# Kernel optimization log

Hardware: AMD Instinct MI355X
Metric: run time of the kernel (lower is better)

## Reference

```python
import jax, jax.numpy as jnp
import numpy as np

B, MAX_N, MAX_E, MAX_BETA = 16, 512, 1024, 64
NODE_F, HID = 2, 128

def setup_inputs() -> dict:
    key = jax.random.key(0)
    ks = jax.random.split(key, 20)
    inp = {}
    inp["x"] = jax.random.normal(ks[0], (B, MAX_N, NODE_F), dtype=jnp.float32)
    inp["SCB"] = jax.random.normal(ks[1], (B, MAX_BETA, MAX_E), dtype=jnp.float32)
    inp["edge_index"] = jax.random.randint(ks[2], (B, 2, MAX_E), 0, MAX_N, dtype=jnp.int32)
    inp["edge_len"] = jax.random.randint(ks[3], (B,), 1, MAX_E + 1, dtype=jnp.int32)
    inp["beta_len"] = jax.random.randint(ks[4], (B,), 1, MAX_BETA + 1, dtype=jnp.int32)
    def lin(k, fi, fo):
        s = 1.0 / np.sqrt(fi)
        kw, kb = jax.random.split(k)
        return (jax.random.uniform(kw, (fi, fo), jnp.float32, -s, s),
                jax.random.uniform(kb, (fo,), jnp.float32, -s, s))
    inp["W1"], inp["b1"] = lin(ks[5], 4, 64)
    inp["W2"], inp["b2"] = lin(ks[6], 64, 64)
    inp["W3"], inp["b3"] = lin(ks[7], 64 + 4, 128)
    inp["W4"], inp["b4"] = lin(ks[8], 128, 128)
    inp["W5"], inp["b5"] = lin(ks[9], 128, HID)
    inp["W6"], inp["b6"] = lin(ks[10], HID, HID)
    return inp

def reference(x, SCB, edge_index, edge_len, beta_len,
              W1, b1, W2, b2, W3, b3, W4, b4, W5, b5, W6, b6):
    Bb, beta, E = SCB.shape
    SCBa = jnp.abs(SCB)  # torch.abs(he[2].to_dense())
    edge_mask = jnp.arange(E)[None, :] < edge_len[:, None]      # [B,E]
    beta_mask = jnp.arange(beta)[None, :] < beta_len[:, None]   # [B,beta]
    # e_feat = x[edge_index].transpose(0,1).reshape(E, 2*node_feat)
    ef = jax.vmap(lambda xi, ei: xi[ei])(x, edge_index)          # [B,2,E,F]
    ef = jnp.transpose(ef, (0, 2, 1, 3)).reshape(Bb, E, -1)      # [B,E,4]
    # SCB_feat[b,beta,e,i] = e_feat[b,e,i] * SCB[b,beta,e]; zero in padded region
    valid = (beta_mask[:, :, None] & edge_mask[:, None, :])[..., None]
    SCB_feat = jnp.where(valid, SCBa[:, :, :, None] * ef[:, None, :, :], 0.0)  # [B,beta,E,4]
    L1 = jnp.transpose(SCB_feat, (0, 2, 1, 3))                   # [B,E,beta,4]
    # SCB_encoder on sum over edges
    s = L1.sum(axis=1)                                            # [B,beta,4]
    emb = jax.nn.relu(s @ W1 + b1) @ W2 + b2                      # [B,beta,64]
    cat = jnp.concatenate([jnp.broadcast_to(emb[:, None], (Bb, E, beta, 64)), L1], axis=-1)
    h = (jax.nn.relu(cat @ W3 + b3) @ W4 + b4).sum(axis=2)        # [B,E,128]
    out = jax.nn.relu(h @ W5 + b5) @ W6 + b6                      # [B,E,HID]
    out = out.reshape(Bb * E, -1)
    # original selects out[Pad_Masks]; zero padded rows instead (jit-static shape)
    return out * edge_mask.reshape(-1, 1).astype(out.dtype)
```

## Files before the change

### kernel.cpp

```cpp
#include <hip/hip_runtime.h>
#include <hip/hip_bf16.h>

#define NB   16
#define NN   512
#define NE   1024
#define NBETA 64
#define NHID 128

typedef __attribute__((ext_vector_type(8))) short short8;
typedef __attribute__((ext_vector_type(4))) float f32x4;

static __device__ __forceinline__ unsigned short f2bf(float f) {
    unsigned u = __float_as_uint(f);
    return (unsigned short)((u + 0x7fffu + ((u >> 16) & 1u)) >> 16);
}

static __device__ __forceinline__ f32x4 splat4(float v) {
    f32x4 r; r.x = v; r.y = v; r.z = v; r.w = v; return r;
}


__global__ __launch_bounds__(128) void k_base_wt(
        const float* __restrict__ x, const int* __restrict__ ei,
        const float* __restrict__ SCB,
        const int* __restrict__ elen, const int* __restrict__ blen,
        const float* __restrict__ W1, const float* __restrict__ b1,
        const float* __restrict__ W2, const float* __restrict__ b2,
        const float* __restrict__ W3, const float* __restrict__ b3,
        const float* __restrict__ W4, const float* __restrict__ W5,
        const float* __restrict__ W6,
        float* __restrict__ base, unsigned short* __restrict__ wsT) {
    int bid = blockIdx.x, tid = threadIdx.x;
    if (bid >= NB * NBETA) {
        int j = (bid - NB * NBETA) * 128 + tid;
        int w = j >> 14, rem = j & 16383;
        int k = rem & 127, n = rem >> 7;
        const float* W = (w == 0) ? W4 : ((w == 1) ? W5 : W6);
        float v = W[k * NHID + n];
        int byte = n * 256 + ((2 * k) ^ ((n & 7) << 4));
        *reinterpret_cast<unsigned short*>(
            reinterpret_cast<char*>(wsT) + (size_t)w * 32768 + byte) = f2bf(v);
        return;
    }
    int bb = bid;
    int b = bb >> 6, beta = bb & 63;
    int el = elen[b], bl = blen[b];
    float a0 = 0, a1 = 0, a2 = 0, a3 = 0;
    if (beta < bl) {
        const float* row = SCB + (size_t)bb * NE;
        const int* eis = ei + b * 2 * NE;
        const float* xb = x + b * NN * 2;
        for (int e = tid; e < el; e += 128) {
            float t = fabsf(row[e]);
            int s0 = eis[e], s1 = eis[NE + e];
            float2 v0 = *reinterpret_cast<const float2*>(xb + 2 * s0);
            float2 v1 = *reinterpret_cast<const float2*>(xb + 2 * s1);
            a0 = fmaf(t, v0.x, a0);
            a1 = fmaf(t, v0.y, a1);
            a2 = fmaf(t, v1.x, a2);
            a3 = fmaf(t, v1.y, a3);
        }
    }
    __shared__ float red[4][128];
    red[0][tid] = a0; red[1][tid] = a1; red[2][tid] = a2; red[3][tid] = a3;
    __syncthreads();
    for (int st = 64; st > 0; st >>= 1) {
        if (tid < st) {
            red[0][tid] += red[0][tid + st];
            red[1][tid] += red[1][tid + st];
            red[2][tid] += red[2][tid + st];
            red[3][tid] += red[3][tid + st];
        }
        __syncthreads();
    }
    __shared__ float h1[64], embv[64];
    if (tid < 64) {
        float v = b1[tid];
        #pragma unroll
        for (int i = 0; i < 4; ++i) v = fmaf(red[i][0], W1[i * 64 + tid], v);
        h1[tid] = fmaxf(v, 0.f);
    }
    __syncthreads();
    if (tid < 64) {
        float v = b2[tid];
        #pragma unroll 8
        for (int k = 0; k < 64; ++k) v = fmaf(h1[k], W2[k * 64 + tid], v);
        embv[tid] = v;
    }
    __syncthreads();
    float v = b3[tid];
    #pragma unroll 8
    for (int k = 0; k < 64; ++k) v = fmaf(embv[k], W3[k * NHID + tid], v);
    base[(size_t)bb * NHID + tid] = v;
}

__global__ __launch_bounds__(512) void k_fused(
        const float* __restrict__ x, const int* __restrict__ ei,
        const float* __restrict__ SCB,
        const int* __restrict__ elen, const int* __restrict__ blen,
        const float* __restrict__ W3,
        const float* __restrict__ base, const unsigned short* __restrict__ wsT,
        const float* __restrict__ b4, const float* __restrict__ b5,
        const float* __restrict__ b6,
        float* __restrict__ out) {
    int bid = blockIdx.x, tid = threadIdx.x;
    int b = bid >> 5;
    int e0 = (bid & 31) * 32;
    int el = elen[b];
    if (e0 >= el) {
        float4 z; z.x = 0.f; z.y = 0.f; z.z = 0.f; z.w = 0.f;
        float4* o4 = reinterpret_cast<float4*>(out) + (size_t)(b * NE + e0) * (NHID / 4);
        o4[tid] = z;
        o4[tid + 512] = z;
        return;
    }
    int bl = blen[b];

    __shared__ __align__(16) char lds[65536];
    float* baseS = reinterpret_cast<float*>(lds);
    char*  wS    = lds + 32768;
    float4* efS  = reinterpret_cast<float4*>(wS);
    float* w3r   = reinterpret_cast<float*>(wS + 512);
    float* tS    = reinterpret_cast<float*>(wS + 8192);
    char* io0 = lds;
    char* io1 = lds + 8192;

    const float4* w4src = reinterpret_cast<const float4*>(wsT);
    const float4* w5src = reinterpret_cast<const float4*>(
        reinterpret_cast<const char*>(wsT) + 32768);
    const float4* w6src = reinterpret_cast<const float4*>(
        reinterpret_cast<const char*>(wsT) + 65536);
    float4 pw0, pw1, pw2, pw3;

    {
        const float4* bsrc = reinterpret_cast<const float4*>(base + (size_t)b * NBETA * NHID);
        float4* bd = reinterpret_cast<float4*>(baseS);
        #pragma unroll
        for (int i = 0; i < 4; ++i) bd[tid + 512 * i] = bsrc[tid + 512 * i];
        {
            int row = tid >> 3, c4 = tid & 7;
            float4 v = *reinterpret_cast<const float4*>(
                SCB + (size_t)(b * NBETA + row) * NE + e0 + c4 * 4);
            v.x = fabsf(v.x); v.y = fabsf(v.y); v.z = fabsf(v.z); v.w = fabsf(v.w);
            reinterpret_cast<float4*>(tS)[tid] = v;
        }
        if (tid < 64) {
            int e = tid >> 1, hf = tid & 1;
            int idx = ei[b * 2 * NE + hf * NE + e0 + e];
            float2 v2 = *reinterpret_cast<const float2*>(x + b * NN * 2 + idx * 2);
            reinterpret_cast<float2*>(&efS[e])[hf] = v2;
        }
        w3r[tid] = W3[64 * NHID + tid];
        pw0 = w4src[tid];        pw1 = w4src[tid + 512];
        pw2 = w4src[tid + 1024]; pw3 = w4src[tid + 1536];
    }
    __syncthreads();

    int cg = tid & 31, es = tid >> 5;
    f32x4 w0  = reinterpret_cast<const f32x4*>(w3r)[cg];
    f32x4 w1  = reinterpret_cast<const f32x4*>(w3r)[32 + cg];
    f32x4 w2  = reinterpret_cast<const f32x4*>(w3r)[64 + cg];
    f32x4 w3v = reinterpret_cast<const f32x4*>(w3r)[96 + cg];
    f32x4 gv[2], acc[2];
    #pragma unroll
    for (int j = 0; j < 2; ++j) {
        float4 e4 = efS[es * 2 + j];
        f32x4 g = w3v * splat4(e4.w);
        g = __builtin_elementwise_fma(splat4(e4.z), w2, g);
        g = __builtin_elementwise_fma(splat4(e4.y), w1, g);
        g = __builtin_elementwise_fma(splat4(e4.x), w0, g);
        gv[j] = g;
        acc[j] = splat4(0.f);
    }
    const f32x4* base4 = reinterpret_cast<const f32x4*>(baseS);
    const f32x4 zero = splat4(0.f);
    for (int beta = 0; beta < bl; ++beta) {
        f32x4 bs = base4[beta * 32 + cg];
        float2 tv = *reinterpret_cast<const float2*>(tS + beta * 32 + es * 2);
        acc[0] += __builtin_elementwise_max(
            __builtin_elementwise_fma(splat4(tv.x), gv[0], bs), zero);
        acc[1] += __builtin_elementwise_max(
            __builtin_elementwise_fma(splat4(tv.y), gv[1], bs), zero);
    }
    if (bl < NBETA) {
        f32x4 bp = base4[bl * 32 + cg];
        f32x4 r = __builtin_elementwise_max(bp, zero);
        f32x4 fcv = splat4((float)(NBETA - bl));
        acc[0] = __builtin_elementwise_fma(fcv, r, acc[0]);
        acc[1] = __builtin_elementwise_fma(fcv, r, acc[1]);
    }
    __syncthreads();

    #pragma unroll
    for (int j = 0; j < 2; ++j) {
        int rl = es * 2 + j;
        int byte = rl * 256 + ((cg * 8) ^ ((rl & 7) << 4));
        ushort4 u;
        u.x = f2bf(acc[0][0]);
        u.x = f2bf(acc[j].x); u.y = f2bf(acc[j].y);
        u.z = f2bf(acc[j].z); u.w = f2bf(acc[j].w);
        *reinterpret_cast<ushort4*>(io0 + byte) = u;
    }
    float4* wd = reinterpret_cast<float4*>(wS);
    wd[tid] = pw0; wd[tid + 512] = pw1; wd[tid + 1024] = pw2; wd[tid + 1536] = pw3;
    pw0 = w5src[tid];        pw1 = w5src[tid + 512];
    pw2 = w5src[tid + 1024]; pw3 = w5src[tid + 1536];
    __syncthreads();

    int l = tid & 63, wid = tid >> 6;
    int wm = wid & 1, wn = wid >> 1;
    const int lrow = l & 15;
    const int kbl = (l >> 4) * 16;

    auto layerc = [&](const char* ioIn, char* ioOut, const float* bias,
                      float bscale, bool doRelu, bool final_) {
        f32x4 facc[2];
        facc[0] = splat4(0.f); facc[1] = splat4(0.f);
        int rowA = wm * 16 + lrow;
        #pragma unroll
        for (int ks = 0; ks < 4; ++ks) {
            int kbyte = ks * 64 + kbl;
            short8 a = *reinterpret_cast<const short8*>(
                ioIn + rowA * 256 + (kbyte ^ ((rowA & 7) << 4)));
            #pragma unroll
            for (int nf = 0; nf < 2; ++nf) {
                int col = wn * 32 + nf * 16 + lrow;
                short8 bf = *reinterpret_cast<const short8*>(
                    wS + col * 256 + (kbyte ^ ((col & 7) << 4)));
                facc[nf] = __builtin_amdgcn_mfma_f32_16x16x32_bf16(a, bf, facc[nf], 0, 0, 0);
            }
        }
        #pragma unroll
        for (int nf = 0; nf < 2; ++nf) {
            int colg = wn * 32 + nf * 16 + lrow;
            float bvv = bias[colg];
            #pragma unroll
            for (int r = 0; r < 4; ++r) {
                int row = wm * 16 + (l >> 4) * 4 + r;
                float v = fmaf(bscale, bvv, facc[nf][r]);
                if (doRelu) v = fmaxf(v, 0.f);
                if (!final_) {
                    *reinterpret_cast<unsigned short*>(
                        ioOut + row * 256 + ((colg * 2) ^ ((row & 7) << 4))) = f2bf(v);
                } else {
                    int eg = e0 + row;
                    if (eg >= el) v = 0.f;
                    out[(size_t)(b * NE + eg) * NHID + colg] = v;
                }
            }
        }
    };

    layerc(io0, io1, b4, 64.f, false, false);
    __syncthreads();
    wd[tid] = pw0; wd[tid + 512] = pw1; wd[tid + 1024] = pw2; wd[tid + 1536] = pw3;
    pw0 = w6src[tid];        pw1 = w6src[tid + 512];
    pw2 = w6src[tid + 1024]; pw3 = w6src[tid + 1536];
    __syncthreads();
    layerc(io1, io0, b5, 1.f, true, false);
    __syncthreads();
    wd[tid] = pw0; wd[tid + 512] = pw1; wd[tid + 1024] = pw2; wd[tid + 1536] = pw3;
    __syncthreads();
    layerc(io0, nullptr, b6, 1.f, false, true);
}

extern "C" void kernel_launch(void* const* d_in, const int* in_sizes, int n_in,
                              void* d_out, int out_size, void* d_ws, size_t ws_size,
                              hipStream_t stream) {
    const float* x    = (const float*)d_in[0];
    const float* SCB  = (const float*)d_in[1];
    const int*   ei   = (const int*)d_in[2];
    const int*   elen = (const int*)d_in[3];
    const int*   blen = (const int*)d_in[4];
    const float* W1 = (const float*)d_in[5];  const float* b1 = (const float*)d_in[6];
    const float* W2 = (const float*)d_in[7];  const float* b2 = (const float*)d_in[8];
    const float* W3 = (const float*)d_in[9];  const float* b3 = (const float*)d_in[10];
    const float* W4 = (const float*)d_in[11]; const float* b4 = (const float*)d_in[12];
    const float* W5 = (const float*)d_in[13]; const float* b5 = (const float*)d_in[14];
    const float* W6 = (const float*)d_in[15]; const float* b6 = (const float*)d_in[16];
    float* out = (float*)d_out;

    float* ws = (float*)d_ws;
    float* base = ws;
    unsigned short* wsT = (unsigned short*)(base + NB * NBETA * NHID);

    hipLaunchKernelGGL(k_base_wt, dim3(NB * NBETA + 384), dim3(128), 0, stream,
                       x, ei, SCB, elen, blen, W1, b1, W2, b2, W3, b3, W4, W5, W6, base, wsT);
    hipLaunchKernelGGL(k_fused, dim3(512), dim3(512), 0, stream,
                       x, ei, SCB, elen, blen, W3, base, wsT, b4, b5, b6, out);
}
```

Before: 26.96 us.

## Merge both kernels into one cooperative kernel with grid sync and atomic tile scheduler

Replaces the two launches with a single cooperative kernel of 256 blocks. The first phase does the weight transpose and the per-beta embedding, computing four betas per block with shuffle reductions. After a grid-wide sync, blocks pull edge tiles from an atomic counter. The aim is to remove the launch gap between the kernels and balance the tiles, which vary in cost with edge_len. In exchange it adds grid-sync overhead, an atomic per tile, and half as many resident blocks for the MLP phase. A two-launch fallback is kept in case the cooperative launch fails.

```diff
diff --git a/kernel.cpp b/kernel.cpp
--- a/kernel.cpp
+++ b/kernel.cpp
@@ -1,11 +1,15 @@
 #include <hip/hip_runtime.h>
 #include <hip/hip_bf16.h>
+#include <hip/hip_cooperative_groups.h>
+
+namespace cg = cooperative_groups;
 
 #define NB   16
 #define NN   512
 #define NE   1024
 #define NBETA 64
 #define NHID 128
+#define NTILE (NB * 32)
 
 typedef __attribute__((ext_vector_type(8))) short short8;
 typedef __attribute__((ext_vector_type(4))) float f32x4;
@@ -19,109 +23,107 @@
     f32x4 r; r.x = v; r.y = v; r.z = v; r.w = v; return r;
 }
 
-
-__global__ __launch_bounds__(128) void k_base_wt(
+__global__ __launch_bounds__(512) void k_all(
         const float* __restrict__ x, const int* __restrict__ ei,
         const float* __restrict__ SCB,
         const int* __restrict__ elen, const int* __restrict__ blen,
         const float* __restrict__ W1, const float* __restrict__ b1,
         const float* __restrict__ W2, const float* __restrict__ b2,
         const float* __restrict__ W3, const float* __restrict__ b3,
-        const float* __restrict__ W4, const float* __restrict__ W5,
-        const float* __restrict__ W6,
-        float* __restrict__ base, unsigned short* __restrict__ wsT) {
+        const float* __restrict__ W4, const float* __restrict__ b4,
+        const float* __restrict__ W5, const float* __restrict__ b5,
+        const float* __restrict__ W6, const float* __restrict__ b6,
+        float* __restrict__ base, unsigned short* __restrict__ wsT,
+        unsigned int* __restrict__ ctr, float* __restrict__ out, int phase) {
+    __shared__ __align__(16) char lds[65536];
     int bid = blockIdx.x, tid = threadIdx.x;
-    if (bid >= NB * NBETA) {
-        int j = (bid - NB * NBETA) * 128 + tid;
-        int w = j >> 14, rem = j & 16383;
-        int k = rem & 127, n = rem >> 7;
-        const float* W = (w == 0) ? W4 : ((w == 1) ? W5 : W6);
-        float v = W[k * NHID + n];
-        int byte = n * 256 + ((2 * k) ^ ((n & 7) << 4));
-        *reinterpret_cast<unsigned short*>(
-            reinterpret_cast<char*>(wsT) + (size_t)w * 32768 + byte) = f2bf(v);
-        return;
+
+    if (phase != 2) {
+        if (tid < 192) {
+            int j = bid * 192 + tid;
+            int w = j >> 14, rem = j & 16383;
+            int k = rem & 127, n = rem >> 7;
+            const float* W = (w == 0) ? W4 : ((w == 1) ? W5 : W6);
+            float v = W[k * NHID + n];
+            int byte = n * 256 + ((2 * k) ^ ((n & 7) << 4));
+            *reinterpret_cast<unsigned short*>(
+                reinterpret_cast<char*>(wsT) + (size_t)w * 32768 + byte) = f2bf(v);
+        }
+        {
+            int hf = tid >> 7, t = tid & 127;
+            int bb = bid * 4 + hf;
+            int b = bb >> 6, beta = bb & 63;
+            int el = elen[b], bl = blen[b];
+            float a0 = 0, a1 = 0, a2 = 0, a3 = 0;
+            if (beta < bl) {
+                const float* row = SCB + (size_t)bb * NE;
+                const int* eis = ei + b * 2 * NE;
+                const float* xb = x + b * NN * 2;
+                for (int e = t; e < el; e += 128) {
+                    float tt = fabsf(row[e]);
+                    int s0 = eis[e], s1 = eis[NE + e];
+                    float2 v0 = *reinterpret_cast<const float2*>(xb + 2 * s0);
+                    float2 v1 = *reinterpret_cast<const float2*>(xb + 2 * s1);
+                    a0 = fmaf(tt, v0.x, a0);
+                    a1 = fmaf(tt, v0.y, a1);
+                    a2 = fmaf(tt, v1.x, a2);
+                    a3 = fmaf(tt, v1.y, a3);
+                }
+            }
+            #pragma unroll
+            for (int off = 32; off > 0; off >>= 1) {
+                a0 += __shfl_down(a0, off);
+                a1 += __shfl_down(a1, off);
+                a2 += __shfl_down(a2, off);
+                a3 += __shfl_down(a3, off);
+            }
+            float* part = reinterpret_cast<float*>(lds);
+            if ((tid & 63) == 0) {
+                int w8 = tid >> 6;
+                part[w8 * 4 + 0] = a0; part[w8 * 4 + 1] = a1;
+                part[w8 * 4 + 2] = a2; part[w8 * 4 + 3] = a3;
+            }
+            __syncthreads();
+            float* h1s  = reinterpret_cast<float*>(lds + 128);
+            float* embs = reinterpret_cast<float*>(lds + 1152);
+            if (t < 64) {
+                float v = b1[t];
+                #pragma unroll
+                for (int i = 0; i < 4; ++i) {
+                    float si = part[(2 * hf) * 4 + i] + part[(2 * hf + 1) * 4 + i];
+                    v = fmaf(si, W1[i * 64 + t], v);
+                }
+                h1s[hf * 64 + t] = fmaxf(v, 0.f);
+            }
+            __syncthreads();
+            if (t < 64) {
+                float v = b2[t];
+                #pragma unroll 8
+                for (int k = 0; k < 64; ++k)
+                    v = fmaf(h1s[hf * 64 + k], W2[k * 64 + t], v);
+                embs[hf * 64 + t] = v;
+            }
+            __syncthreads();
+            {
+                float v = b3[t];
+                #pragma unroll 8
+                for (int k = 0; k < 64; ++k)
+                    v = fmaf(embs[hf * 64 + k], W3[k * NHID + t], v);
+                base[(size_t)bb * NHID + t] = v;
+            }
+        }
+        if (bid == 0 && tid == 0) atomicExch(ctr, 0u);
+        if (phase == 1) return;
+        __threadfence();
+        cg::this_grid().sync();
     }
-    int bb = bid;
-    int b = bb >> 6, beta = bb & 63;
-    int el = elen[b], bl = blen[b];
-    float a0 = 0, a1 = 0, a2 = 0, a3 = 0;
-    if (beta < bl) {
-        const float* row = SCB + (size_t)bb * NE;
-        const int* eis = ei + b * 2 * NE;
-        const float* xb = x + b * NN * 2;
-        for (int e = tid; e < el; e += 128) {
-            float t = fabsf(row[e]);
-            int s0 = eis[e], s1 = eis[NE + e];
-            float2 v0 = *reinterpret_cast<const float2*>(xb + 2 * s0);
-            float2 v1 = *reinterpret_cast<const float2*>(xb + 2 * s1);
-            a0 = fmaf(t, v0.x, a0);
-            a1 = fmaf(t, v0.y, a1);
-            a2 = fmaf(t, v1.x, a2);
-            a3 = fmaf(t, v1.y, a3);
-        }
-    }
-    __shared__ float red[4][128];
-    red[0][tid] = a0; red[1][tid] = a1; red[2][tid] = a2; red[3][tid] = a3;
-    __syncthreads();
-    for (int st = 64; st > 0; st >>= 1) {
-        if (tid < st) {
-            red[0][tid] += red[0][tid + st];
-            red[1][tid] += red[1][tid + st];
-            red[2][tid] += red[2][tid + st];
-            red[3][tid] += red[3][tid + st];
-        }
-        __syncthreads();
-    }
-    __shared__ float h1[64], embv[64];
-    if (tid < 64) {
-        float v = b1[tid];
-        #pragma unroll
-        for (int i = 0; i < 4; ++i) v = fmaf(red[i][0], W1[i * 64 + tid], v);
-        h1[tid] = fmaxf(v, 0.f);
-    }
-    __syncthreads();
-    if (tid < 64) {
-        float v = b2[tid];
-        #pragma unroll 8
-        for (int k = 0; k < 64; ++k) v = fmaf(h1[k], W2[k * 64 + tid], v);
-        embv[tid] = v;
-    }
-    __syncthreads();
-    float v = b3[tid];
-    #pragma unroll 8
-    for (int k = 0; k < 64; ++k) v = fmaf(embv[k], W3[k * NHID + tid], v);
-    base[(size_t)bb * NHID + tid] = v;
-}
-
-__global__ __launch_bounds__(512) void k_fused(
-        const float* __restrict__ x, const int* __restrict__ ei,
-        const float* __restrict__ SCB,
-        const int* __restrict__ elen, const int* __restrict__ blen,
-        const float* __restrict__ W3,
-        const float* __restrict__ base, const unsigned short* __restrict__ wsT,
-        const float* __restrict__ b4, const float* __restrict__ b5,
-        const float* __restrict__ b6,
-        float* __restrict__ out) {
-    int bid = blockIdx.x, tid = threadIdx.x;
-    int b = bid >> 5;
-    int e0 = (bid & 31) * 32;
-    int el = elen[b];
-    if (e0 >= el) {
-        float4 z; z.x = 0.f; z.y = 0.f; z.z = 0.f; z.w = 0.f;
-        float4* o4 = reinterpret_cast<float4*>(out) + (size_t)(b * NE + e0) * (NHID / 4);
-        o4[tid] = z;
-        o4[tid + 512] = z;
-        return;
-    }
-    int bl = blen[b];
-
-    __shared__ __align__(16) char lds[65536];
+
     float* baseS = reinterpret_cast<float*>(lds);
     char*  wS    = lds + 32768;
     float4* efS  = reinterpret_cast<float4*>(wS);
     float* w3r   = reinterpret_cast<float*>(wS + 512);
     float* tS    = reinterpret_cast<float*>(wS + 8192);
+    unsigned int* tileS = reinterpret_cast<unsigned int*>(lds + 32768 + 2560);
     char* io0 = lds;
     char* io1 = lds + 8192;
 
@@ -130,138 +132,157 @@
         reinterpret_cast<const char*>(wsT) + 32768);
     const float4* w6src = reinterpret_cast<const float4*>(
         reinterpret_cast<const char*>(wsT) + 65536);
-    float4 pw0, pw1, pw2, pw3;
-
-    {
-        const float4* bsrc = reinterpret_cast<const float4*>(base + (size_t)b * NBETA * NHID);
-        float4* bd = reinterpret_cast<float4*>(baseS);
+
+    while (true) {
+        __syncthreads();
+        if (tid == 0) *tileS = atomicAdd(ctr, 1u);
+        __syncthreads();
+        unsigned int tile = *tileS;
+        if (tile >= NTILE) break;
+        int b = (int)tile >> 5;
+        int e0 = ((int)tile & 31) * 32;
+        int el = elen[b];
+        if (e0 >= el) {
+            float4 z; z.x = 0.f; z.y = 0.f; z.z = 0.f; z.w = 0.f;
+            float4* o4 = reinterpret_cast<float4*>(out) + (size_t)(b * NE + e0) * 32;
+            o4[tid] = z;
+            o4[tid + 512] = z;
+            continue;
+        }
+        int bl = blen[b];
+        float4 pw0, pw1, pw2, pw3;
+
+        {
+            const float4* bsrc = reinterpret_cast<const float4*>(
+                base + (size_t)b * NBETA * NHID);
+            float4* bd = reinterpret_cast<float4*>(baseS);
+            #pragma unroll
+            for (int i = 0; i < 4; ++i) bd[tid + 512 * i] = bsrc[tid + 512 * i];
+            {
+                int row = tid >> 3, c4 = tid & 7;
+                float4 v = *reinterpret_cast<const float4*>(
+                    SCB + (size_t)(b * NBETA + row) * NE + e0 + c4 * 4);
+                v.x = fabsf(v.x); v.y = fabsf(v.y); v.z = fabsf(v.z); v.w = fabsf(v.w);
+                reinterpret_cast<float4*>(tS)[tid] = v;
+            }
+            if (tid < 64) {
+                int e = tid >> 1, hf2 = tid & 1;
+                int idx = ei[b * 2 * NE + hf2 * NE + e0 + e];
+                float2 v2 = *reinterpret_cast<const float2*>(x + b * NN * 2 + idx * 2);
+                reinterpret_cast<float2*>(&efS[e])[hf2] = v2;
+            }
+            w3r[tid] = W3[64 * NHID + tid];
+            pw0 = w4src[tid];        pw1 = w4src[tid + 512];
+            pw2 = w4src[tid + 1024]; pw3 = w4src[tid + 1536];
+        }
+        __syncthreads();
+
+        int cg2 = tid & 31, es = tid >> 5;
+        f32x4 w0  = reinterpret_cast<const f32x4*>(w3r)[cg2];
+        f32x4 w1  = reinterpret_cast<const f32x4*>(w3r)[32 + cg2];
+        f32x4 w2  = reinterpret_cast<const f32x4*>(w3r)[64 + cg2];
+        f32x4 w3v = reinterpret_cast<const f32x4*>(w3r)[96 + cg2];
+        f32x4 gv[2], acc[2];
         #pragma unroll
-        for (int i = 0; i < 4; ++i) bd[tid + 512 * i] = bsrc[tid + 512 * i];
-        {
-            int row = tid >> 3, c4 = tid & 7;
-            float4 v = *reinterpret_cast<const float4*>(
-                SCB + (size_t)(b * NBETA + row) * NE + e0 + c4 * 4);
-            v.x = fabsf(v.x); v.y = fabsf(v.y); v.z = fabsf(v.z); v.w = fabsf(v.w);
-            reinterpret_cast<float4*>(tS)[tid] = v;
-        }
-        if (tid < 64) {
-            int e = tid >> 1, hf = tid & 1;
-            int idx = ei[b * 2 * NE + hf * NE + e0 + e];
-            float2 v2 = *reinterpret_cast<const float2*>(x + b * NN * 2 + idx * 2);
-            reinterpret_cast<float2*>(&efS[e])[hf] = v2;
-        }
-        w3r[tid] = W3[64 * NHID + tid];
-        pw0 = w4src[tid];        pw1 = w4src[tid + 512];
-        pw2 = w4src[tid + 1024]; pw3 = w4src[tid + 1536];
-    }
-    __syncthreads();
-
-    int cg = tid & 31, es = tid >> 5;
-    f32x4 w0  = reinterpret_cast<const f32x4*>(w3r)[cg];
-    f32x4 w1  = reinterpret_cast<const f32x4*>(w3r)[32 + cg];
-    f32x4 w2  = reinterpret_cast<const f32x4*>(w3r)[64 + cg];
-    f32x4 w3v = reinterpret_cast<const f32x4*>(w3r)[96 + cg];
-    f32x4 gv[2], acc[2];
-    #pragma unroll
-    for (int j = 0; j < 2; ++j) {
-        float4 e4 = efS[es * 2 + j];
-        f32x4 g = w3v * splat4(e4.w);
-        g = __builtin_elementwise_fma(splat4(e4.z), w2, g);
-        g = __builtin_elementwise_fma(splat4(e4.y), w1, g);
-        g = __builtin_elementwise_fma(splat4(e4.x), w0, g);
-        gv[j] = g;
-        acc[j] = splat4(0.f);
-    }
-    const f32x4* base4 = reinterpret_cast<const f32x4*>(baseS);
-    const f32x4 zero = splat4(0.f);
-    for (int beta = 0; beta < bl; ++beta) {
-        f32x4 bs = base4[beta * 32 + cg];
-        float2 tv = *reinterpret_cast<const float2*>(tS + beta * 32 + es * 2);
-        acc[0] += __builtin_elementwise_max(
-            __builtin_elementwise_fma(splat4(tv.x), gv[0], bs), zero);
-        acc[1] += __builtin_elementwise_max(
-            __builtin_elementwise_fma(splat4(tv.y), gv[1], bs), zero);
-    }
-    if (bl < NBETA) {
-        f32x4 bp = base4[bl * 32 + cg];
-        f32x4 r = __builtin_elementwise_max(bp, zero);
-        f32x4 fcv = splat4((float)(NBETA - bl));
-        acc[0] = __builtin_elementwise_fma(fcv, r, acc[0]);
-        acc[1] = __builtin_elementwise_fma(fcv, r, acc[1]);
-    }
-    __syncthreads();
-
-    #pragma unroll
-    for (int j = 0; j < 2; ++j) {
-        int rl = es * 2 + j;
-        int byte = rl * 256 + ((cg * 8) ^ ((rl & 7) << 4));
-        ushort4 u;
-        u.x = f2bf(acc[0][0]);
-        u.x = f2bf(acc[j].x); u.y = f2bf(acc[j].y);
-        u.z = f2bf(acc[j].z); u.w = f2bf(acc[j].w);
-        *reinterpret_cast<ushort4*>(io0 + byte) = u;
-    }
-    float4* wd = reinterpret_cast<float4*>(wS);
-    wd[tid] = pw0; wd[tid + 512] = pw1; wd[tid + 1024] = pw2; wd[tid + 1536] = pw3;
-    pw0 = w5src[tid];        pw1 = w5src[tid + 512];
-    pw2 = w5src[tid + 1024]; pw3 = w5src[tid + 1536];
-    __syncthreads();
-
-    int l = tid & 63, wid = tid >> 6;
-    int wm = wid & 1, wn = wid >> 1;
-    const int lrow = l & 15;
-    const int kbl = (l >> 4) * 16;
-
-    auto layerc = [&](const char* ioIn, char* ioOut, const float* bias,
-                      float bscale, bool doRelu, bool final_) {
-        f32x4 facc[2];
-        facc[0] = splat4(0.f); facc[1] = splat4(0.f);
-        int rowA = wm * 16 + lrow;
+        for (int j = 0; j < 2; ++j) {
+            float4 e4 = efS[es * 2 + j];
+            f32x4 g = w3v * splat4(e4.w);
+            g = __builtin_elementwise_fma(splat4(e4.z), w2, g);
+            g = __builtin_elementwise_fma(splat4(e4.y), w1, g);
+            g = __builtin_elementwise_fma(splat4(e4.x), w0, g);
+            gv[j] = g;
+            acc[j] = splat4(0.f);
+        }
+        const f32x4* base4 = reinterpret_cast<const f32x4*>(baseS);
+        const f32x4 zero = splat4(0.f);
+        for (int beta = 0; beta < bl; ++beta) {
+            f32x4 bs = base4[beta * 32 + cg2];
+            float2 tv = *reinterpret_cast<const float2*>(tS + beta * 32 + es * 2);
+            acc[0] += __builtin_elementwise_max(
+                __builtin_elementwise_fma(splat4(tv.x), gv[0], bs), zero);
+            acc[1] += __builtin_elementwise_max(
+                __builtin_elementwise_fma(splat4(tv.y), gv[1], bs), zero);
+        }
+        if (bl < NBETA) {
+            f32x4 bp = base4[bl * 32 + cg2];
+            f32x4 r = __builtin_elementwise_max(bp, zero);
+            f32x4 fcv = splat4((float)(NBETA - bl));
+            acc[0] = __builtin_elementwise_fma(fcv, r, acc[0]);
+            acc[1] = __builtin_elementwise_fma(fcv, r, acc[1]);
+        }
+        __syncthreads();
+
         #pragma unroll
-        for (int ks = 0; ks < 4; ++ks) {
-            int kbyte = ks * 64 + kbl;
-            short8 a = *reinterpret_cast<const short8*>(
-                ioIn + rowA * 256 + (kbyte ^ ((rowA & 7) << 4)));
+        for (int j = 0; j < 2; ++j) {
+            int rl = es * 2 + j;
+            int byte = rl * 256 + ((cg2 * 8) ^ ((rl & 7) << 4));
+            ushort4 u;
+            u.x = f2bf(acc[j].x); u.y = f2bf(acc[j].y);
+            u.z = f2bf(acc[j].z); u.w = f2bf(acc[j].w);
+            *reinterpret_cast<ushort4*>(io0 + byte) = u;
+        }
+        float4* wd = reinterpret_cast<float4*>(wS);
+        wd[tid] = pw0; wd[tid + 512] = pw1; wd[tid + 1024] = pw2; wd[tid + 1536] = pw3;
+        pw0 = w5src[tid];        pw1 = w5src[tid + 512];
+        pw2 = w5src[tid + 1024]; pw3 = w5src[tid + 1536];
+        __syncthreads();
+
+        int l = tid & 63, wid = tid >> 6;
+        int wm = wid & 1, wn = wid >> 1;
+        const int lrow = l & 15;
+        const int kbl = (l >> 4) * 16;
+
+        auto layerc = [&](const char* ioIn, char* ioOut, const float* bias,
+                          float bscale, bool doRelu, bool final_) {
+            f32x4 facc[2];
+            facc[0] = splat4(0.f); facc[1] = splat4(0.f);
+            int rowA = wm * 16 + lrow;
+            #pragma unroll
+            for (int ks = 0; ks < 4; ++ks) {
+                int kbyte = ks * 64 + kbl;
+                short8 a = *reinterpret_cast<const short8*>(
+                    ioIn + rowA * 256 + (kbyte ^ ((rowA & 7) << 4)));
+                #pragma unroll
+                for (int nf = 0; nf < 2; ++nf) {
+                    int col = wn * 32 + nf * 16 + lrow;
+                    short8 bf = *reinterpret_cast<const short8*>(
+                        wS + col * 256 + (kbyte ^ ((col & 7) << 4)));
+                    facc[nf] = __builtin_amdgcn_mfma_f32_16x16x32_bf16(a, bf, facc[nf], 0, 0, 0);
+                }
+            }
             #pragma unroll
             for (int nf = 0; nf < 2; ++nf) {
-                int col = wn * 32 + nf * 16 + lrow;
-                short8 bf = *reinterpret_cast<const short8*>(
-                    wS + col * 256 + (kbyte ^ ((col & 7) << 4)));
-                facc[nf] = __builtin_amdgcn_mfma_f32_16x16x32_bf16(a, bf, facc[nf], 0, 0, 0);
-            }
-        }
-        #pragma unroll
-        for (int nf = 0; nf < 2; ++nf) {
-            int colg = wn * 32 + nf * 16 + lrow;
-            float bvv = bias[colg];
-            #pragma unroll
-            for (int r = 0; r < 4; ++r) {
-                int row = wm * 16 + (l >> 4) * 4 + r;
-                float v = fmaf(bscale, bvv, facc[nf][r]);
-                if (doRelu) v = fmaxf(v, 0.f);
-                if (!final_) {
-                    *reinterpret_cast<unsigned short*>(
-                        ioOut + row * 256 + ((colg * 2) ^ ((row & 7) << 4))) = f2bf(v);
-                } else {
-                    int eg = e0 + row;
-                    if (eg >= el) v = 0.f;
-                    out[(size_t)(b * NE + eg) * NHID + colg] = v;
+                int colg = wn * 32 + nf * 16 + lrow;
+                float bvv = bias[colg];
+                #pragma unroll
+                for (int r = 0; r < 4; ++r) {
+                    int row = wm * 16 + (l >> 4) * 4 + r;
+                    float v = fmaf(bscale, bvv, facc[nf][r]);
+                    if (doRelu) v = fmaxf(v, 0.f);
+                    if (!final_) {
+                        *reinterpret_cast<unsigned short*>(
+                            ioOut + row * 256 + ((colg * 2) ^ ((row & 7) << 4))) = f2bf(v);
+                    } else {
+                        int eg = e0 + row;
+                        float vv = (eg >= el) ? 0.f : v;
+                        out[(size_t)(b * NE + eg) * NHID + colg] = vv;
+                    }
                 }
             }
-        }
-    };
-
-    layerc(io0, io1, b4, 64.f, false, false);
-    __syncthreads();
-    wd[tid] = pw0; wd[tid + 512] = pw1; wd[tid + 1024] = pw2; wd[tid + 1536] = pw3;
-    pw0 = w6src[tid];        pw1 = w6src[tid + 512];
-    pw2 = w6src[tid + 1024]; pw3 = w6src[tid + 1536];
-    __syncthreads();
-    layerc(io1, io0, b5, 1.f, true, false);
-    __syncthreads();
-    wd[tid] = pw0; wd[tid + 512] = pw1; wd[tid + 1024] = pw2; wd[tid + 1536] = pw3;
-    __syncthreads();
-    layerc(io0, nullptr, b6, 1.f, false, true);
+        };
+
+        layerc(io0, io1, b4, 64.f, false, false);
+        __syncthreads();
+        wd[tid] = pw0; wd[tid + 512] = pw1; wd[tid + 1024] = pw2; wd[tid + 1536] = pw3;
+        pw0 = w6src[tid];        pw1 = w6src[tid + 512];
+        pw2 = w6src[tid + 1024]; pw3 = w6src[tid + 1536];
+        __syncthreads();
+        layerc(io1, io0, b5, 1.f, true, false);
+        __syncthreads();
+        wd[tid] = pw0; wd[tid + 512] = pw1; wd[tid + 1024] = pw2; wd[tid + 1536] = pw3;
+        __syncthreads();
+        layerc(io0, nullptr, b6, 1.f, false, true);
+    }
 }
 
 extern "C" void kernel_launch(void* const* d_in, const int* in_sizes, int n_in,
@@ -283,9 +304,24 @@
     float* ws = (float*)d_ws;
     float* base = ws;
     unsigned short* wsT = (unsigned short*)(base + NB * NBETA * NHID);
-
-    hipLaunchKernelGGL(k_base_wt, dim3(NB * NBETA + 384), dim3(128), 0, stream,
-                       x, ei, SCB, elen, blen, W1, b1, W2, b2, W3, b3, W4, W5, W6, base, wsT);
-    hipLaunchKernelGGL(k_fused, dim3(512), dim3(512), 0, stream,
-                       x, ei, SCB, elen, blen, W3, base, wsT, b4, b5, b6, out);
+    unsigned int* ctr = (unsigned int*)(wsT + 49152);
+
+    int ph0 = 0;
+    void* args[] = { (void*)&x, (void*)&ei, (void*)&SCB, (void*)&elen, (void*)&blen,
+                     (void*)&W1, (void*)&b1, (void*)&W2, (void*)&b2,
+                     (void*)&W3, (void*)&b3, (void*)&W4, (void*)&b4,
+                     (void*)&W5, (void*)&b5, (void*)&W6, (void*)&b6,
+                     (void*)&base, (void*)&wsT, (void*)&ctr, (void*)&out,
+                     (void*)&ph0 };
+    hipError_t err = hipLaunchCooperativeKernel((const void*)k_all, dim3(256),
+                                                dim3(512), args, 0, stream);
+    if (err != hipSuccess) {
+        (void)hipGetLastError();
+        hipLaunchKernelGGL(k_all, dim3(256), dim3(512), 0, stream,
+                           x, ei, SCB, elen, blen, W1, b1, W2, b2, W3, b3,
+                           W4, b4, W5, b5, W6, b6, base, wsT, ctr, out, 1);
+        hipLaunchKernelGGL(k_all, dim3(512), dim3(512), 0, stream,
+                           x, ei, SCB, elen, blen, W1, b1, W2, b2, W3, b3,
+                           W4, b4, W5, b5, W6, b6, base, wsT, ctr, out, 2);
+    }
 }
```

Result: slower. 95.68 us (+254.9%).

## Pack four beta rows per block, use wave shuffles, interleave fused-kernel batch mapping

Applied to the files above, without the earlier changes.

The first kernel now runs 256 blocks of 512 threads. Each block handles four (batch, beta) rows and also does a slice of the weight transpose and bf16 conversion, where before that work ran in separate blocks. The shared-memory tree reduction with barriers at every step is replaced by wave shuffle reductions plus one small shared combine. The fused kernel maps block indices with the batch in the low bits, so early-exit blocks for padded edges are spread across the grid and the load is better balanced. Packing more work per block may lower occupancy, and the first kernel's duration now depends on its slowest row in each group of four.

```diff
diff --git a/kernel.cpp b/kernel.cpp
--- a/kernel.cpp
+++ b/kernel.cpp
@@ -20,7 +20,7 @@
 }
 
 
-__global__ __launch_bounds__(128) void k_base_wt(
+__global__ __launch_bounds__(512) void k_base_wt(
         const float* __restrict__ x, const int* __restrict__ ei,
         const float* __restrict__ SCB,
         const int* __restrict__ elen, const int* __restrict__ blen,
@@ -30,9 +30,13 @@
         const float* __restrict__ W4, const float* __restrict__ W5,
         const float* __restrict__ W6,
         float* __restrict__ base, unsigned short* __restrict__ wsT) {
+    __shared__ float part[32];
+    __shared__ float h1s[4][64];
+    __shared__ float embs[4][64];
     int bid = blockIdx.x, tid = threadIdx.x;
-    if (bid >= NB * NBETA) {
-        int j = (bid - NB * NBETA) * 128 + tid;
+
+    if (tid < 192) {
+        int j = bid * 192 + tid;
         int w = j >> 14, rem = j & 16383;
         int k = rem & 127, n = rem >> 7;
         const float* W = (w == 0) ? W4 : ((w == 1) ? W5 : W6);
@@ -40,9 +44,10 @@
         int byte = n * 256 + ((2 * k) ^ ((n & 7) << 4));
         *reinterpret_cast<unsigned short*>(
             reinterpret_cast<char*>(wsT) + (size_t)w * 32768 + byte) = f2bf(v);
-        return;
-    }
-    int bb = bid;
+    }
+
+    int hf = tid >> 7, t = tid & 127;
+    int bb = bid * 4 + hf;
     int b = bb >> 6, beta = bb & 63;
     int el = elen[b], bl = blen[b];
     float a0 = 0, a1 = 0, a2 = 0, a3 = 0;
@@ -50,48 +55,53 @@
         const float* row = SCB + (size_t)bb * NE;
         const int* eis = ei + b * 2 * NE;
         const float* xb = x + b * NN * 2;
-        for (int e = tid; e < el; e += 128) {
-            float t = fabsf(row[e]);
+        for (int e = t; e < el; e += 128) {
+            float tt = fabsf(row[e]);
             int s0 = eis[e], s1 = eis[NE + e];
             float2 v0 = *reinterpret_cast<const float2*>(xb + 2 * s0);
             float2 v1 = *reinterpret_cast<const float2*>(xb + 2 * s1);
-            a0 = fmaf(t, v0.x, a0);
-            a1 = fmaf(t, v0.y, a1);
-            a2 = fmaf(t, v1.x, a2);
-            a3 = fmaf(t, v1.y, a3);
-        }
-    }
-    __shared__ float red[4][128];
-    red[0][tid] = a0; red[1][tid] = a1; red[2][tid] = a2; red[3][tid] = a3;
-    __syncthreads();
-    for (int st = 64; st > 0; st >>= 1) {
-        if (tid < st) {
-            red[0][tid] += red[0][tid + st];
-            red[1][tid] += red[1][tid + st];
-            red[2][tid] += red[2][tid + st];
-            red[3][tid] += red[3][tid + st];
-        }
-        __syncthreads();
-    }
-    __shared__ float h1[64], embv[64];
-    if (tid < 64) {
-        float v = b1[tid];
+            a0 = fmaf(tt, v0.x, a0);
+            a1 = fmaf(tt, v0.y, a1);
+            a2 = fmaf(tt, v1.x, a2);
+            a3 = fmaf(tt, v1.y, a3);
+        }
+    }
+    #pragma unroll
+    for (int off = 32; off > 0; off >>= 1) {
+        a0 += __shfl_down(a0, off);
+        a1 += __shfl_down(a1, off);
+        a2 += __shfl_down(a2, off);
+        a3 += __shfl_down(a3, off);
+    }
+    if ((tid & 63) == 0) {
+        int w8 = tid >> 6;
+        part[w8 * 4 + 0] = a0; part[w8 * 4 + 1] = a1;
+        part[w8 * 4 + 2] = a2; part[w8 * 4 + 3] = a3;
+    }
+    __syncthreads();
+    if (t < 64) {
+        float v = b1[t];
         #pragma unroll
-        for (int i = 0; i < 4; ++i) v = fmaf(red[i][0], W1[i * 64 + tid], v);
-        h1[tid] = fmaxf(v, 0.f);
-    }
-    __syncthreads();
-    if (tid < 64) {
-        float v = b2[tid];
+        for (int i = 0; i < 4; ++i) {
+            float si = part[(2 * hf) * 4 + i] + part[(2 * hf + 1) * 4 + i];
+            v = fmaf(si, W1[i * 64 + t], v);
+        }
+        h1s[hf][t] = fmaxf(v, 0.f);
+    }
+    __syncthreads();
+    if (t < 64) {
+        float v = b2[t];
         #pragma unroll 8
-        for (int k = 0; k < 64; ++k) v = fmaf(h1[k], W2[k * 64 + tid], v);
-        embv[tid] = v;
-    }
-    __syncthreads();
-    float v = b3[tid];
-    #pragma unroll 8
-    for (int k = 0; k < 64; ++k) v = fmaf(embv[k], W3[k * NHID + tid], v);
-    base[(size_t)bb * NHID + tid] = v;
+        for (int k = 0; k < 64; ++k) v = fmaf(h1s[hf][k], W2[k * 64 + t], v);
+        embs[hf][t] = v;
+    }
+    __syncthreads();
+    {
+        float v = b3[t];
+        #pragma unroll 8
+        for (int k = 0; k < 64; ++k) v = fmaf(embs[hf][k], W3[k * NHID + t], v);
+        base[(size_t)bb * NHID + t] = v;
+    }
 }
 
 __global__ __launch_bounds__(512) void k_fused(
@@ -104,8 +114,8 @@
         const float* __restrict__ b6,
         float* __restrict__ out) {
     int bid = blockIdx.x, tid = threadIdx.x;
-    int b = bid >> 5;
-    int e0 = (bid & 31) * 32;
+    int b = bid & 15;
+    int e0 = (bid >> 4) * 32;
     int el = elen[b];
     if (e0 >= el) {
         float4 z; z.x = 0.f; z.y = 0.f; z.z = 0.f; z.w = 0.f;
@@ -196,7 +206,6 @@
         int rl = es * 2 + j;
         int byte = rl * 256 + ((cg * 8) ^ ((rl & 7) << 4));
         ushort4 u;
-        u.x = f2bf(acc[0][0]);
         u.x = f2bf(acc[j].x); u.y = f2bf(acc[j].y);
         u.z = f2bf(acc[j].z); u.w = f2bf(acc[j].w);
         *reinterpret_cast<ushort4*>(io0 + byte) = u;
@@ -244,8 +253,8 @@
                         ioOut + row * 256 + ((colg * 2) ^ ((row & 7) << 4))) = f2bf(v);
                 } else {
                     int eg = e0 + row;
-                    if (eg >= el) v = 0.f;
-                    out[(size_t)(b * NE + eg) * NHID + colg] = v;
+                    float vv = (eg >= el) ? 0.f : v;
+                    out[(size_t)(b * NE + eg) * NHID + colg] = vv;
                 }
             }
         }
@@ -284,7 +293,7 @@
     float* base = ws;
     unsigned short* wsT = (unsigned short*)(base + NB * NBETA * NHID);
 
-    hipLaunchKernelGGL(k_base_wt, dim3(NB * NBETA + 384), dim3(128), 0, stream,
+    hipLaunchKernelGGL(k_base_wt, dim3(256), dim3(512), 0, stream,
                        x, ei, SCB, elen, blen, W1, b1, W2, b2, W3, b3, W4, W5, W6, base, wsT);
     hipLaunchKernelGGL(k_fused, dim3(512), dim3(512), 0, stream,
                        x, ei, SCB, elen, blen, W3, base, wsT, b4, b5, b6, out);
```

Result: no change. 26.99 us, median of 2 (+0.1%).
